# Kernel optimization log

Hardware: AMD Instinct MI355X
Metric: run time of the kernel (lower is better)

Reference implementation:

```python
import jax, jax.numpy as jnp
import numpy as np

N_NODES = 50000
N_EDGES = 800000
HID = 256
OUT = 128
NEG_SLOPE = 0.2


def gat_layer(x, src, dst, W_src, W_dst, a_src_vec, a_dst_vec, bias, n_nodes):
    # Dense projections (PyG lin_src / lin_dst for tuple in_channels)
    h_src = x @ W_src              # [N, C]
    h_dst = x @ W_dst              # [N, C]
    # Per-node attention logits (att_src/att_dst dot products)
    a_src = h_src @ a_src_vec      # [N]
    a_dst = h_dst @ a_dst_vec      # [N]
    # Edge logits + LeakyReLU
    e = jax.nn.leaky_relu(a_src[src] + a_dst[dst], NEG_SLOPE)  # [E]
    # Segment softmax over incoming edges of each dst node
    m = jax.ops.segment_max(e, dst, num_segments=n_nodes)      # [N]
    m = jnp.where(jnp.isfinite(m), m, 0.0)                      # empty segments
    ex = jnp.exp(e - m[dst])                                    # [E]
    s = jax.ops.segment_sum(ex, dst, num_segments=n_nodes)     # [N]
    alpha = ex / (s[dst] + 1e-16)                               # [E]
    # Attention-weighted message aggregation (scatter-add to dst)
    msg = alpha[:, None] * h_src[src]                           # [E, C]
    out = jax.ops.segment_sum(msg, dst, num_segments=n_nodes)  # [N, C]
    return out + bias


def setup_inputs() -> dict:
    key = jax.random.key(0)
    ks = jax.random.split(key, 12)
    x = jax.random.normal(ks[0], (N_NODES, HID), dtype=jnp.float32)
    edge_index = jax.random.randint(ks[1], (2, N_EDGES), 0, N_NODES, dtype=jnp.int64)
    sc1 = 1.0 / np.sqrt(HID)
    sc2 = 1.0 / np.sqrt(HID)
    return {
        "x": x,
        "edge_index": edge_index,
        "W1_src": jax.random.normal(ks[2], (HID, HID), dtype=jnp.float32) * sc1,
        "W1_dst": jax.random.normal(ks[3], (HID, HID), dtype=jnp.float32) * sc1,
        "att1_src": jax.random.normal(ks[4], (HID,), dtype=jnp.float32) * sc1,
        "att1_dst": jax.random.normal(ks[5], (HID,), dtype=jnp.float32) * sc1,
        "b1": jnp.zeros((HID,), dtype=jnp.float32),
        "W2_src": jax.random.normal(ks[6], (HID, OUT), dtype=jnp.float32) * sc2,
        "W2_dst": jax.random.normal(ks[7], (HID, OUT), dtype=jnp.float32) * sc2,
        "att2_src": jax.random.normal(ks[8], (OUT,), dtype=jnp.float32) * (1.0 / np.sqrt(OUT)),
        "att2_dst": jax.random.normal(ks[9], (OUT,), dtype=jnp.float32) * (1.0 / np.sqrt(OUT)),
        "b2": jnp.zeros((OUT,), dtype=jnp.float32),
    }


def reference(x, edge_index, W1_src, W1_dst, att1_src, att1_dst, b1,
              W2_src, W2_dst, att2_src, att2_dst, b2):
    src, dst = edge_index[0], edge_index[1]
    h = gat_layer(x, src, dst, W1_src, W1_dst, att1_src, att1_dst, b1, N_NODES)
    h = jax.nn.relu(h)
    out = gat_layer(h, src, dst, W2_src, W2_dst, att2_src, att2_dst, b2, N_NODES)
    return out
```

## Files before the change

### kernel.cpp

```cpp
#include <hip/hip_runtime.h>
#include <math.h>

#define N_NODES 50000
#define N_EDGES 800000
#define HID 256
#define OUT_C 128
#define NEG_SLOPE 0.2f
#define SCAN_NB ((N_NODES + 255) / 256)

typedef __attribute__((ext_vector_type(8))) short bf16x8;
typedef __attribute__((ext_vector_type(4))) float f32x4;
typedef _Float16 half_t;
typedef __attribute__((ext_vector_type(4))) _Float16 half4;
typedef __attribute__((ext_vector_type(2))) _Float16 half2t;

__device__ inline unsigned short bf16_rne(float x) {
    unsigned u = __float_as_uint(x);
    return (unsigned short)((u + 0x7fffu + ((u >> 16) & 1u)) >> 16);
}


__global__ __launch_bounds__(256) void hist_rank_kernel(
    const int* __restrict__ dst, int* __restrict__ counts, int* __restrict__ rank) {
    int e = blockIdx.x * 256 + threadIdx.x;
    if (e < N_EDGES) rank[e] = atomicAdd(&counts[dst[e]], 1);
}

__global__ __launch_bounds__(256) void block_scan_kernel(
    const int* __restrict__ counts, int* __restrict__ excl,
    int* __restrict__ blockSums, int n) {
    __shared__ int waveSums[4];
    int i = blockIdx.x * 256 + threadIdx.x;
    int lane = threadIdx.x & 63;
    int wv = threadIdx.x >> 6;
    int c = (i < n) ? counts[i] : 0;
    int v = c;
    #pragma unroll
    for (int off = 1; off < 64; off <<= 1) {
        int t = __shfl_up(v, off);
        if (lane >= off) v += t;
    }
    if (lane == 63) waveSums[wv] = v;
    __syncthreads();
    int waveOff = 0;
    #pragma unroll
    for (int w = 0; w < 4; w++)
        if (w < wv) waveOff += waveSums[w];
    if (i < n) excl[i] = waveOff + v - c;
    if (threadIdx.x == 255) blockSums[blockIdx.x] = waveOff + v;
}

__global__ __launch_bounds__(256) void add_offsets_kernel(
    int* __restrict__ excl, const int* __restrict__ blockSums, int n) {
    __shared__ int lds[4];
    int tid = threadIdx.x;
    int partial = 0;
    for (int j = tid; j < (int)blockIdx.x; j += 256) partial += blockSums[j];
    #pragma unroll
    for (int off = 32; off > 0; off >>= 1) partial += __shfl_down(partial, off);
    if ((tid & 63) == 0) lds[tid >> 6] = partial;
    __syncthreads();
    int prefix = lds[0] + lds[1] + lds[2] + lds[3];
    int i = blockIdx.x * 256 + tid;
    if (i < n) excl[i] += prefix;
    if (i == 0) excl[n] = N_EDGES;
}

__global__ __launch_bounds__(256) void scatter_kernel(
    const int* __restrict__ src, const int* __restrict__ dst,
    const int* __restrict__ offsets, const int* __restrict__ rank,
    int* __restrict__ src_sorted) {
    int e = blockIdx.x * 256 + threadIdx.x;
    if (e >= N_EDGES) return;
    src_sorted[offsets[dst[e]] + rank[e]] = src[e];
}


__global__ __launch_bounds__(64) void compute_v_all_kernel(
    const float* __restrict__ W1s, const float* __restrict__ att1s,
    const float* __restrict__ W1d, const float* __restrict__ att1d,
    const float* __restrict__ W2s, const float* __restrict__ att2s,
    const float* __restrict__ W2d, const float* __restrict__ att2d,
    float* __restrict__ v1s, float* __restrict__ v1d,
    float* __restrict__ v2s, float* __restrict__ v2d) {
    int k = blockIdx.x;
    int lane = threadIdx.x;
    const float* W; const float* att; float* v; int cout;
    switch (blockIdx.y) {
        case 0: W = W1s; att = att1s; v = v1s; cout = HID; break;
        case 1: W = W1d; att = att1d; v = v1d; cout = HID; break;
        case 2: W = W2s; att = att2s; v = v2s; cout = OUT_C; break;
        default: W = W2d; att = att2d; v = v2d; cout = OUT_C; break;
    }
    float sum = 0.f;
    for (int j = lane; j < cout; j += 64)
        sum += W[k * cout + j] * att[j];
    #pragma unroll
    for (int off = 32; off > 0; off >>= 1)
        sum += __shfl_down(sum, off);
    if (lane == 0) v[k] = sum;
}


#define PACK1_T (8 * 17 * 64)
#define PACK2_T (8 * 9 * 64)

__global__ __launch_bounds__(256) void pack_all_kernel(
    const float* __restrict__ W1, const float* __restrict__ v1s, const float* __restrict__ v1d,
    const float* __restrict__ W2, const float* __restrict__ v2s, const float* __restrict__ v2d,
    unsigned short* __restrict__ hi1, unsigned short* __restrict__ lo1,
    unsigned short* __restrict__ hi2, unsigned short* __restrict__ lo2) {
    int t = blockIdx.x * 256 + threadIdx.x;
    const float *W, *vs, *vd; unsigned short *hi, *lo; int cout, NTL, tt;
    if (t < PACK1_T)            { tt = t;           W = W1; vs = v1s; vd = v1d; hi = hi1; lo = lo1; cout = HID;  NTL = 17; }
    else if (t < PACK1_T + PACK2_T) { tt = t - PACK1_T; W = W2; vs = v2s; vd = v2d; hi = hi2; lo = lo2; cout = OUT_C; NTL = 9; }
    else return;
    int lane = tt & 63;
    int tile = (tt >> 6) % NTL;
    int ks = tt / (64 * NTL);
    int m = lane & 15;
    int kbase = ks * 32 + (lane >> 4) * 8;
    #pragma unroll
    for (int j = 0; j < 8; j++) {
        float val;
        if (tile < NTL - 1) val = W[(kbase + j) * cout + tile * 16 + m];
        else val = (m == 0) ? vs[kbase + j] : (m == 1) ? vd[kbase + j] : 0.f;
        unsigned short h = bf16_rne(val);
        hi[tt * 8 + j] = h;
        lo[tt * 8 + j] = bf16_rne(val - __uint_as_float((unsigned)h << 16));
    }
}


template <int COUT, int NT, bool WRITE_A>
__device__ __forceinline__ void gemm_body(
    const float* __restrict__ A, const unsigned short* __restrict__ Bhi,
    const unsigned short* __restrict__ Blo, half_t* __restrict__ H,
    float* __restrict__ a_s, float* __restrict__ a_d, int M, int tile0) {
    const int NTL = COUT / 16 + 1;
    int wave = threadIdx.x >> 6, lane = threadIdx.x & 63;
    int m = lane & 15, quad = lane >> 4;
    int row0 = blockIdx.x * 128 + wave * 32;
    f32x4 acc[2][NT];
    #pragma unroll
    for (int rg = 0; rg < 2; rg++)
        #pragma unroll
        for (int nt = 0; nt < NT; nt++)
            acc[rg][nt] = (f32x4){0.f, 0.f, 0.f, 0.f};

    const float* arow[2];
    #pragma unroll
    for (int rg = 0; rg < 2; rg++) {
        int r = row0 + rg * 16 + m;
        if (r >= M) r = M - 1;
        arow[rg] = A + (size_t)r * HID;
    }

    for (int ks = 0; ks < 8; ks++) {
        bf16x8 ah[2], al[2];
        #pragma unroll
        for (int rg = 0; rg < 2; rg++) {
            const float* ap = arow[rg] + ks * 32 + quad * 8;
            float4 v0 = *(const float4*)ap;
            float4 v1 = *(const float4*)(ap + 4);
            float av[8] = {v0.x, v0.y, v0.z, v0.w, v1.x, v1.y, v1.z, v1.w};
            #pragma unroll
            for (int j = 0; j < 8; j++) {
                unsigned short h = bf16_rne(av[j]);
                float hf = __uint_as_float((unsigned)h << 16);
                ah[rg][j] = (short)h;
                al[rg][j] = (short)bf16_rne(av[j] - hf);
            }
        }
        #pragma unroll
        for (int nt = 0; nt < NT; nt++) {
            int tile = (WRITE_A && nt == NT - 1) ? (COUT / 16) : (tile0 + nt);
            size_t fbase = ((size_t)(ks * NTL + tile) * 64 + lane) * 8;
            bf16x8 bh = *(const bf16x8*)(Bhi + fbase);
            bf16x8 bl = *(const bf16x8*)(Blo + fbase);
            acc[0][nt] = __builtin_amdgcn_mfma_f32_16x16x32_bf16(ah[0], bh, acc[0][nt], 0, 0, 0);
            acc[1][nt] = __builtin_amdgcn_mfma_f32_16x16x32_bf16(ah[1], bh, acc[1][nt], 0, 0, 0);
            acc[0][nt] = __builtin_amdgcn_mfma_f32_16x16x32_bf16(ah[0], bl, acc[0][nt], 0, 0, 0);
            acc[1][nt] = __builtin_amdgcn_mfma_f32_16x16x32_bf16(ah[1], bl, acc[1][nt], 0, 0, 0);
            acc[0][nt] = __builtin_amdgcn_mfma_f32_16x16x32_bf16(al[0], bh, acc[0][nt], 0, 0, 0);
            acc[1][nt] = __builtin_amdgcn_mfma_f32_16x16x32_bf16(al[1], bh, acc[1][nt], 0, 0, 0);
        }
    }
    const int NW = WRITE_A ? NT - 1 : NT;
    #pragma unroll
    for (int rg = 0; rg < 2; rg++)
        #pragma unroll
        for (int nt = 0; nt < NW; nt++)
            #pragma unroll
            for (int r = 0; r < 4; r++) {
                int row = row0 + rg * 16 + quad * 4 + r;
                if (row < M)
                    H[(size_t)row * COUT + (tile0 + nt) * 16 + m] = (half_t)acc[rg][nt][r];
            }
    if (WRITE_A) {
        #pragma unroll
        for (int rg = 0; rg < 2; rg++)
            #pragma unroll
            for (int r = 0; r < 4; r++) {
                int row = row0 + rg * 16 + quad * 4 + r;
                if (row < M) {
                    if (m == 0) a_s[row] = acc[rg][NT - 1][r];
                    else if (m == 1) a_d[row] = acc[rg][NT - 1][r];
                }
            }
    }
}

template <int COUT>
__global__ __launch_bounds__(256) void mfma_gemm_a_kernel(
    const float* __restrict__ A, const unsigned short* __restrict__ Bhi,
    const unsigned short* __restrict__ Blo, half_t* __restrict__ H,
    float* __restrict__ a_s, float* __restrict__ a_d, int M) {
    if (blockIdx.y == 0)
        gemm_body<COUT, 9, true>(A, Bhi, Blo, H, a_s, a_d, M, 0);
    else
        gemm_body<COUT, 8, false>(A, Bhi, Blo, H, a_s, a_d, M, 8);
}


template <int C, bool RELU>
__global__ __launch_bounds__(256) void fused_aggregate_kernel(
    const int* __restrict__ offsets, const int* __restrict__ src_sorted,
    const float* __restrict__ a_src, const float* __restrict__ a_dst,
    const half_t* __restrict__ h, const float* __restrict__ bias,
    float* __restrict__ out) {
    constexpr int CH = 8;
    int node = (int)((blockIdx.x * 256u + threadIdx.x) >> 6);
    int lane = threadIdx.x & 63;
    if (node >= N_NODES) return;
    int beg = offsets[node], end = offsets[node + 1];
    float ad = a_dst[node];
    float s = 0.f;

    if (C == 256) {
        float4 acc = make_float4(0.f, 0.f, 0.f, 0.f);
        for (int base = beg; base < end; base += CH) {
            int cnt = end - base; if (cnt > CH) cnt = CH;
            int idx[CH];
            #pragma unroll
            for (int j = 0; j < CH; j++)
                idx[j] = src_sorted[(j < cnt) ? base + j : base];
            half4 hv[CH];
            #pragma unroll
            for (int j = 0; j < CH; j++)
                hv[j] = *(const half4*)(h + (size_t)idx[j] * C + lane * 4);
            float w[CH];
            #pragma unroll
            for (int j = 0; j < CH; j++) {
                float l = a_src[idx[j]] + ad;
                if (l < 0.f) l *= NEG_SLOPE;
                w[j] = (j < cnt) ? expf(l) : 0.f;
                s += w[j];
            }
            #pragma unroll
            for (int j = 0; j < CH; j++) {
                acc.x += w[j] * (float)hv[j][0]; acc.y += w[j] * (float)hv[j][1];
                acc.z += w[j] * (float)hv[j][2]; acc.w += w[j] * (float)hv[j][3];
            }
        }
        float inv = 1.f / (s + 1e-16f);
        float4 bv = *(const float4*)(bias + lane * 4);
        acc.x = acc.x * inv + bv.x; acc.y = acc.y * inv + bv.y;
        acc.z = acc.z * inv + bv.z; acc.w = acc.w * inv + bv.w;
        if (RELU) {
            acc.x = fmaxf(acc.x, 0.f); acc.y = fmaxf(acc.y, 0.f);
            acc.z = fmaxf(acc.z, 0.f); acc.w = fmaxf(acc.w, 0.f);
        }
        *(float4*)(out + (size_t)node * C + lane * 4) = acc;
    } else {
        float2 acc = make_float2(0.f, 0.f);
        for (int base = beg; base < end; base += CH) {
            int cnt = end - base; if (cnt > CH) cnt = CH;
            int idx[CH];
            #pragma unroll
            for (int j = 0; j < CH; j++)
                idx[j] = src_sorted[(j < cnt) ? base + j : base];
            half2t hv[CH];
            #pragma unroll
            for (int j = 0; j < CH; j++)
                hv[j] = *(const half2t*)(h + (size_t)idx[j] * C + lane * 2);
            float w[CH];
            #pragma unroll
            for (int j = 0; j < CH; j++) {
                float l = a_src[idx[j]] + ad;
                if (l < 0.f) l *= NEG_SLOPE;
                w[j] = (j < cnt) ? expf(l) : 0.f;
                s += w[j];
            }
            #pragma unroll
            for (int j = 0; j < CH; j++) {
                acc.x += w[j] * (float)hv[j][0]; acc.y += w[j] * (float)hv[j][1];
            }
        }
        float inv = 1.f / (s + 1e-16f);
        float2 bv = *(const float2*)(bias + lane * 2);
        acc.x = acc.x * inv + bv.x; acc.y = acc.y * inv + bv.y;
        if (RELU) { acc.x = fmaxf(acc.x, 0.f); acc.y = fmaxf(acc.y, 0.f); }
        *(float2*)(out + (size_t)node * C + lane * 2) = acc;
    }
}

extern "C" void kernel_launch(void* const* d_in, const int* in_sizes, int n_in,
                              void* d_out, int out_size, void* d_ws, size_t ws_size,
                              hipStream_t stream) {
    const float* x     = (const float*)d_in[0];
    const int*   edge  = (const int*)d_in[1];
    const int*   src   = edge;
    const int*   dst   = edge + N_EDGES;
    const float* W1s   = (const float*)d_in[2];
    const float* W1d   = (const float*)d_in[3];
    const float* att1s = (const float*)d_in[4];
    const float* att1d = (const float*)d_in[5];
    const float* b1    = (const float*)d_in[6];
    const float* W2s   = (const float*)d_in[7];
    const float* W2d   = (const float*)d_in[8];
    const float* att2s = (const float*)d_in[9];
    const float* att2d = (const float*)d_in[10];
    const float* b2    = (const float*)d_in[11];
    float* out = (float*)d_out;

    float* ws    = (float*)d_ws;
    half_t* h1   = (half_t*)ws;
    float* act2  = ws + (size_t)N_NODES * HID;
    float* a_s   = act2 + (size_t)N_NODES * HID;
    float* a_d   = a_s + N_NODES;
    float* vbuf  = a_d + N_NODES;
    int* ibase      = (int*)(vbuf + 4 * HID);
    int* src_sorted = ibase;
    int* rank       = src_sorted + N_EDGES;
    int* counts     = rank + N_EDGES;
    int* offsets    = counts + N_NODES;
    int* blockSums  = offsets + N_NODES + 1;
    unsigned short* wp1h = (unsigned short*)(((uintptr_t)(blockSums + SCAN_NB) + 15) & ~(uintptr_t)15);
    unsigned short* wp1l = wp1h + PACK1_T * 8;
    unsigned short* wp2h = wp1l + PACK1_T * 8;
    unsigned short* wp2l = wp2h + PACK2_T * 8;
    float* v1s = vbuf, *v1d = vbuf + HID, *v2s = vbuf + 2 * HID, *v2d = vbuf + 3 * HID;
    half_t* h2 = h1;

    const int edgeBlocks = (N_EDGES + 255) / 256;
    const int waveBlocksN = (N_NODES + 3) / 4;
    const int gemmBlocks = (N_NODES + 127) / 128;

    hipMemsetAsync(counts, 0, N_NODES * sizeof(int), stream);
    hist_rank_kernel<<<edgeBlocks, 256, 0, stream>>>(dst, counts, rank);
    block_scan_kernel<<<SCAN_NB, 256, 0, stream>>>(counts, offsets, blockSums, N_NODES);
    add_offsets_kernel<<<SCAN_NB, 256, 0, stream>>>(offsets, blockSums, N_NODES);
    scatter_kernel<<<edgeBlocks, 256, 0, stream>>>(src, dst, offsets, rank, src_sorted);

    compute_v_all_kernel<<<dim3(HID, 4), 64, 0, stream>>>(
        W1s, att1s, W1d, att1d, W2s, att2s, W2d, att2d, v1s, v1d, v2s, v2d);
    pack_all_kernel<<<(PACK1_T + PACK2_T + 255) / 256, 256, 0, stream>>>(
        W1s, v1s, v1d, W2s, v2s, v2d, wp1h, wp1l, wp2h, wp2l);

    mfma_gemm_a_kernel<HID><<<dim3(gemmBlocks, 2), 256, 0, stream>>>(
        x, wp1h, wp1l, h1, a_s, a_d, N_NODES);
    fused_aggregate_kernel<HID, true><<<waveBlocksN, 256, 0, stream>>>(
        offsets, src_sorted, a_s, a_d, h1, b1, act2);

    mfma_gemm_a_kernel<OUT_C><<<dim3(gemmBlocks, 1), 256, 0, stream>>>(
        act2, wp2h, wp2l, h2, a_s, a_d, N_NODES);
    fused_aggregate_kernel<OUT_C, false><<<waveBlocksN, 256, 0, stream>>>(
        offsets, src_sorted, a_s, a_d, h2, b2, out);
}
```

Measured before the change: 338.1 us.

## Precompute per-edge attention weights into packed CSR (src, weight) array

Replaces the one-time src scatter with a per-layer edge kernel. It computes leaky-ReLU plus exp for each edge and writes the source index and weight as an int2, in CSR order. The aggregation kernels then read these pairs instead of gathering a_src per neighbour and computing exp inline. This takes a dependent random gather and the transcendental work out of the latency-bound aggregation loop. The cost is an extra edge pass per layer, wider scattered writes, and the faster approximate exp.

Measured after the change: 361.9 us. +7.0%, slower.

```diff
diff --git a/kernel.cpp b/kernel.cpp
--- a/kernel.cpp
+++ b/kernel.cpp
@@ -66,13 +66,19 @@
     if (i == 0) excl[n] = N_EDGES;
 }
 
-__global__ __launch_bounds__(256) void scatter_kernel(
+
+__global__ __launch_bounds__(256) void edge_weight_kernel(
     const int* __restrict__ src, const int* __restrict__ dst,
     const int* __restrict__ offsets, const int* __restrict__ rank,
-    int* __restrict__ src_sorted) {
+    const float* __restrict__ a_src, const float* __restrict__ a_dst,
+    int2* __restrict__ ew) {
     int e = blockIdx.x * 256 + threadIdx.x;
     if (e >= N_EDGES) return;
-    src_sorted[offsets[dst[e]] + rank[e]] = src[e];
+    int s = src[e], d = dst[e];
+    float l = a_src[s] + a_dst[d];
+    l = fmaxf(l, l * NEG_SLOPE);
+    float w = __expf(l);
+    ew[offsets[d] + rank[e]] = make_int2(s, __float_as_int(w));
 }
 
 
@@ -225,8 +231,7 @@
 
 template <int C, bool RELU>
 __global__ __launch_bounds__(256) void fused_aggregate_kernel(
-    const int* __restrict__ offsets, const int* __restrict__ src_sorted,
-    const float* __restrict__ a_src, const float* __restrict__ a_dst,
+    const int* __restrict__ offsets, const int2* __restrict__ ew,
     const half_t* __restrict__ h, const float* __restrict__ bias,
     float* __restrict__ out) {
     constexpr int CH = 8;
@@ -234,33 +239,26 @@
     int lane = threadIdx.x & 63;
     if (node >= N_NODES) return;
     int beg = offsets[node], end = offsets[node + 1];
-    float ad = a_dst[node];
     float s = 0.f;
 
     if (C == 256) {
         float4 acc = make_float4(0.f, 0.f, 0.f, 0.f);
         for (int base = beg; base < end; base += CH) {
             int cnt = end - base; if (cnt > CH) cnt = CH;
-            int idx[CH];
+            int2 e[CH];
             #pragma unroll
             for (int j = 0; j < CH; j++)
-                idx[j] = src_sorted[(j < cnt) ? base + j : base];
+                e[j] = ew[(j < cnt) ? base + j : base];
             half4 hv[CH];
             #pragma unroll
             for (int j = 0; j < CH; j++)
-                hv[j] = *(const half4*)(h + (size_t)idx[j] * C + lane * 4);
-            float w[CH];
+                hv[j] = *(const half4*)(h + ((unsigned)e[j].x * C + lane * 4));
             #pragma unroll
             for (int j = 0; j < CH; j++) {
-                float l = a_src[idx[j]] + ad;
-                if (l < 0.f) l *= NEG_SLOPE;
-                w[j] = (j < cnt) ? expf(l) : 0.f;
-                s += w[j];
-            }
-            #pragma unroll
-            for (int j = 0; j < CH; j++) {
-                acc.x += w[j] * (float)hv[j][0]; acc.y += w[j] * (float)hv[j][1];
-                acc.z += w[j] * (float)hv[j][2]; acc.w += w[j] * (float)hv[j][3];
+                float w = (j < cnt) ? __int_as_float(e[j].y) : 0.f;
+                s += w;
+                acc.x += w * (float)hv[j][0]; acc.y += w * (float)hv[j][1];
+                acc.z += w * (float)hv[j][2]; acc.w += w * (float)hv[j][3];
             }
         }
         float inv = 1.f / (s + 1e-16f);
@@ -276,25 +274,19 @@
         float2 acc = make_float2(0.f, 0.f);
         for (int base = beg; base < end; base += CH) {
             int cnt = end - base; if (cnt > CH) cnt = CH;
-            int idx[CH];
+            int2 e[CH];
             #pragma unroll
             for (int j = 0; j < CH; j++)
-                idx[j] = src_sorted[(j < cnt) ? base + j : base];
+                e[j] = ew[(j < cnt) ? base + j : base];
             half2t hv[CH];
             #pragma unroll
             for (int j = 0; j < CH; j++)
-                hv[j] = *(const half2t*)(h + (size_t)idx[j] * C + lane * 2);
-            float w[CH];
+                hv[j] = *(const half2t*)(h + ((unsigned)e[j].x * C + lane * 2));
             #pragma unroll
             for (int j = 0; j < CH; j++) {
-                float l = a_src[idx[j]] + ad;
-                if (l < 0.f) l *= NEG_SLOPE;
-                w[j] = (j < cnt) ? expf(l) : 0.f;
-                s += w[j];
-            }
-            #pragma unroll
-            for (int j = 0; j < CH; j++) {
-                acc.x += w[j] * (float)hv[j][0]; acc.y += w[j] * (float)hv[j][1];
+                float w = (j < cnt) ? __int_as_float(e[j].y) : 0.f;
+                s += w;
+                acc.x += w * (float)hv[j][0]; acc.y += w * (float)hv[j][1];
             }
         }
         float inv = 1.f / (s + 1e-16f);
@@ -326,13 +318,13 @@
 
     float* ws    = (float*)d_ws;
     half_t* h1   = (half_t*)ws;
+    int2* ew     = (int2*)(ws + (size_t)N_NODES * HID / 2);
     float* act2  = ws + (size_t)N_NODES * HID;
     float* a_s   = act2 + (size_t)N_NODES * HID;
     float* a_d   = a_s + N_NODES;
     float* vbuf  = a_d + N_NODES;
     int* ibase      = (int*)(vbuf + 4 * HID);
-    int* src_sorted = ibase;
-    int* rank       = src_sorted + N_EDGES;
+    int* rank       = ibase;
     int* counts     = rank + N_EDGES;
     int* offsets    = counts + N_NODES;
     int* blockSums  = offsets + N_NODES + 1;
@@ -351,7 +343,6 @@
     hist_rank_kernel<<<edgeBlocks, 256, 0, stream>>>(dst, counts, rank);
     block_scan_kernel<<<SCAN_NB, 256, 0, stream>>>(counts, offsets, blockSums, N_NODES);
     add_offsets_kernel<<<SCAN_NB, 256, 0, stream>>>(offsets, blockSums, N_NODES);
-    scatter_kernel<<<edgeBlocks, 256, 0, stream>>>(src, dst, offsets, rank, src_sorted);
 
     compute_v_all_kernel<<<dim3(HID, 4), 64, 0, stream>>>(
         W1s, att1s, W1d, att1d, W2s, att2s, W2d, att2d, v1s, v1d, v2s, v2d);
@@ -360,11 +351,15 @@
 
     mfma_gemm_a_kernel<HID><<<dim3(gemmBlocks, 2), 256, 0, stream>>>(
         x, wp1h, wp1l, h1, a_s, a_d, N_NODES);
+    edge_weight_kernel<<<edgeBlocks, 256, 0, stream>>>(
+        src, dst, offsets, rank, a_s, a_d, ew);
     fused_aggregate_kernel<HID, true><<<waveBlocksN, 256, 0, stream>>>(
-        offsets, src_sorted, a_s, a_d, h1, b1, act2);
+        offsets, ew, h1, b1, act2);
 
     mfma_gemm_a_kernel<OUT_C><<<dim3(gemmBlocks, 1), 256, 0, stream>>>(
         act2, wp2h, wp2l, h2, a_s, a_d, N_NODES);
+    edge_weight_kernel<<<edgeBlocks, 256, 0, stream>>>(
+        src, dst, offsets, rank, a_s, a_d, ew);
     fused_aggregate_kernel<OUT_C, false><<<waveBlocksN, 256, 0, stream>>>(
-        offsets, src_sorted, a_s, a_d, h2, b2, out);
-}
+        offsets, ew, h2, b2, out);
+}
```
